# Optimization experiments

Hardware: AMD Instinct MI355X
Metric: run time of the kernel (lower is better)

The kernel has to match this reference:

```python
import jax, jax.numpy as jnp
import numpy as np

D_MODEL = 1024
N_HEADS = 16
D_KEYS = 64
GROUP_POSITIONS = [list(range(g * 32, (g + 1) * 32)) for g in range(4)]


def _make_tables(group_positions, dim):
    # InGroup table: pe[j,i] = (j/Lg) * L0 / 10000^(2*(i//2)/dim)
    L0 = len(group_positions[0])
    rows = []
    for grp in group_positions:
        Lg = len(grp)
        for j in range(Lg):
            rows.append([j / Lg * L0 / np.power(10000.0, 2 * (i // 2) / dim) for i in range(dim)])
    pe = np.array(rows)
    ingroup = np.concatenate([np.sin(pe[:, 0::2]), np.cos(pe[:, 1::2])], axis=1).astype(np.float32)
    # Sequence (group) table: pe[j,i] = grp[0] / 10000^(j/Lg), constant over i
    rows = []
    for grp in group_positions:
        Lg = len(grp)
        for j in range(Lg):
            rows.append([grp[0] / np.power(10000.0, j / Lg) for _ in range(dim)])
    pe = np.array(rows)
    seq = np.concatenate([np.sin(pe[:, 0::2]), np.cos(pe[:, 1::2])], axis=1).astype(np.float32)
    return jnp.asarray(ingroup), jnp.asarray(seq)


def setup_inputs() -> dict:
    key = jax.random.key(0)
    ks = jax.random.split(key, 12)
    B, L, S = 64, 128, 128
    dqk = D_KEYS * N_HEADS
    sc_in = 1.0 / np.sqrt(D_MODEL)
    sc_out = 1.0 / np.sqrt(dqk)
    inp = {
        "queries": jax.random.normal(ks[0], (B, L, D_MODEL), jnp.float32),
        "keys": jax.random.normal(ks[1], (B, S, D_MODEL), jnp.float32),
        "values": jax.random.normal(ks[2], (B, S, D_MODEL), jnp.float32),
        "attn_mask": jnp.zeros((B, 1, L, S), dtype=bool),
        "Wq": jax.random.normal(ks[3], (D_MODEL, dqk), jnp.float32) * sc_in,
        "bq": jnp.zeros((dqk,), jnp.float32),
        "Wk": jax.random.normal(ks[4], (D_MODEL, dqk), jnp.float32) * sc_in,
        "bk": jnp.zeros((dqk,), jnp.float32),
        "Wv": jax.random.normal(ks[5], (D_MODEL, dqk), jnp.float32) * sc_in,
        "bv": jnp.zeros((dqk,), jnp.float32),
        "Wo": jax.random.normal(ks[6], (dqk, D_MODEL), jnp.float32) * sc_out,
        "bo": jnp.zeros((D_MODEL,), jnp.float32),
    }
    pos_ingroup, pos_seq = _make_tables(GROUP_POSITIONS, D_KEYS)
    inp["pos_ingroup"] = pos_ingroup  # [n_pos, d_keys]
    inp["pos_seq"] = pos_seq          # [n_pos, d_keys]
    return inp


def _rope(x, pos):
    # x: [B, H, L, D]; pos: [L, D]
    sin, cos = jnp.split(pos, 2, axis=-1)
    sin_pos = jnp.stack([sin, sin], axis=-1).reshape(pos.shape)
    cos_pos = jnp.stack([cos, cos], axis=-1).reshape(pos.shape)
    rot = jnp.stack([-x[..., 1::2], x[..., ::2]], axis=-1).reshape(x.shape)
    return x * cos_pos + rot * sin_pos


def reference(queries, keys, values, attn_mask, Wq, bq, Wk, bk, Wv, bv, Wo, bo, pos_ingroup, pos_seq):
    B, L, _ = queries.shape
    S = keys.shape[1]
    H, E = N_HEADS, D_KEYS
    q = (queries @ Wq + bq).reshape(B, L, H, E).transpose(0, 2, 1, 3)  # [B,H,L,E]
    k = (keys @ Wk + bk).reshape(B, S, H, E).transpose(0, 2, 1, 3)
    v = (values @ Wv + bv).reshape(B, S, H, E).transpose(0, 2, 1, 3)
    # group-sequence in-group RoPE, then group RoPE (tables gathered at arange positions)
    q = _rope(_rope(q, pos_ingroup[:L]), pos_seq[:L])
    k = _rope(_rope(k, pos_ingroup[:S]), pos_seq[:S])
    # inner full attention on [B,L,H,E] layout
    scale = 1.0 / jnp.sqrt(jnp.asarray(E, q.dtype))
    scores = jnp.einsum("bhle,bhse->bhls", q, k) * scale
    scores = jnp.where(attn_mask, jnp.asarray(-jnp.inf, scores.dtype), scores)
    attn = jax.nn.softmax(scores, axis=-1)  # [B,H,L,S]
    out = jnp.einsum("bhls,bhsd->blhd", attn, v).reshape(B, L, H * E)
    return out @ Wo + bo, attn
```

## Files before the change

### kernel.cpp

```cpp
#include <hip/hip_runtime.h>
#include <cstdint>

typedef float f32x4 __attribute__((ext_vector_type(4)));
typedef __bf16 bf16x8 __attribute__((ext_vector_type(8)));

typedef __attribute__((address_space(3))) uint32_t lds_u32;
typedef __attribute__((address_space(1))) const uint32_t glb_u32;

#define GLOAD_LDS16(gp, lp) \
  __builtin_amdgcn_global_load_lds((glb_u32*)(uintptr_t)(gp), (lds_u32*)(uintptr_t)(lp), 16, 0, 0)

__device__ inline unsigned short f2bf(float f) {
  union { float f; uint32_t u; } v; v.f = f;
  uint32_t u = v.u;
  return (unsigned short)((u + 0x7fffu + ((u >> 16) & 1u)) >> 16);
}

__global__ void prep_w(const float* __restrict__ wq, const float* __restrict__ wk,
                       const float* __restrict__ wv, const float* __restrict__ wo,
                       unsigned short* __restrict__ wt)
{
  __shared__ float t[64][65];
  const int z = blockIdx.z;
  const float* W = (z == 0) ? wq : (z == 1) ? wk : (z == 2) ? wv : wo;
  unsigned short* Wt = wt + (size_t)z * 1048576;
  const int n0 = blockIdx.x * 64, k0 = blockIdx.y * 64;
  const int tx = threadIdx.x & 63, ty = threadIdx.x >> 6;
#pragma unroll
  for (int i = 0; i < 16; i++) {
    int row = i * 4 + ty;
    t[row][tx] = W[(size_t)(k0 + row) * 1024 + n0 + tx];
  }
  __syncthreads();
#pragma unroll
  for (int i = 0; i < 16; i++) {
    int row = i * 4 + ty;
    Wt[(size_t)(n0 + row) * 1024 + k0 + tx] = f2bf(t[tx][row]);
  }
}

__global__ void comb_kernel(const float* __restrict__ ing, const float* __restrict__ seq,
                            float* __restrict__ cosc, float* __restrict__ sinc)
{
  int idx = blockIdx.x * 256 + threadIdx.x;
  int j = idx >> 5, i = idx & 31;
  float s1 = ing[j * 64 + i], c1 = ing[j * 64 + 32 + i];
  float s2 = seq[j * 64 + i], c2 = seq[j * 64 + 32 + i];
  cosc[idx] = c1 * c2 - s1 * s2;
  sinc[idx] = s1 * c2 + c1 * s2;
}

__global__ void cvt_kernel(const float* __restrict__ q, const float* __restrict__ k,
                           const float* __restrict__ v, unsigned short* __restrict__ dst)
{
  const int z = blockIdx.z;
  const float* src = (z == 0) ? q : (z == 1) ? k : v;
  unsigned short* d = dst + (size_t)z * 8388608;
  size_t i = ((size_t)blockIdx.x * 256 + threadIdx.x) * 4;
  float4 f = *(const float4*)&src[i];
  ushort4 o;
  o.x = f2bf(f.x); o.y = f2bf(f.y); o.z = f2bf(f.z); o.w = f2bf(f.w);
  *(ushort4*)&d[i] = o;
}

__global__ __launch_bounds__(256, 2)
void gemm_bt(const unsigned short* __restrict__ Abase,
             const unsigned short* __restrict__ Bbase,
             const float* __restrict__ b0, const float* __restrict__ b1,
             const float* __restrict__ b2,
             unsigned short* __restrict__ qb, unsigned short* __restrict__ kb,
             unsigned short* __restrict__ vtb,
             float* __restrict__ outf,
             const float* __restrict__ cosc, const float* __restrict__ sinc,
             int final_mode)
{
  __shared__ __attribute__((aligned(16))) unsigned short As[128 * 64];
  __shared__ __attribute__((aligned(16))) unsigned short Bs[128 * 64];

  const int tid = threadIdx.x;
  const int lane = tid & 63;
  const int wave = tid >> 6;
  const int quad = lane >> 4;
  const int l15 = lane & 15;

  const int z = blockIdx.z;
  const int tileM = blockIdx.x * 128;
  const int tileN = blockIdx.y * 128;
  const int K = 1024;

  const unsigned short* A = Abase + (size_t)z * (8192u * 1024u);
  const unsigned short* B = Bbase + (size_t)z * (1024u * 1024u);

  const int wm = (wave >> 1) * 64;
  const int wn = (wave & 1) * 64;

  f32x4 acc[4][4];
#pragma unroll
  for (int a = 0; a < 4; a++)
#pragma unroll
    for (int n = 0; n < 4; n++)
      acc[a][n] = (f32x4){0.f, 0.f, 0.f, 0.f};

  for (int k0 = 0; k0 < K; k0 += 64) {
#pragma unroll
    for (int cc = 0; cc < 4; cc++) {
      int c = wave * 4 + cc;
      int s = c * 64 + lane;
      int row = s >> 3;
      int gc = (s & 7) ^ (row & 7);
      const unsigned short* ga = A + (size_t)(tileM + row) * K + k0 + gc * 8;
      const unsigned short* gb = B + (size_t)(tileN + row) * K + k0 + gc * 8;
      GLOAD_LDS16(ga, &As[c * 512]);
      GLOAD_LDS16(gb, &Bs[c * 512]);
    }
    __syncthreads();

#pragma unroll
    for (int ks = 0; ks < 2; ks++) {
      bf16x8 af[4], bfr[4];
#pragma unroll
      for (int a = 0; a < 4; a++) {
        int r = wm + a * 16 + l15;
        int cp = (ks * 4 + quad) ^ (r & 7);
        af[a] = *(const bf16x8*)&As[(r * 8 + cp) * 8];
      }
#pragma unroll
      for (int n = 0; n < 4; n++) {
        int r = wn + n * 16 + l15;
        int cp = (ks * 4 + quad) ^ (r & 7);
        bfr[n] = *(const bf16x8*)&Bs[(r * 8 + cp) * 8];
      }
#pragma unroll
      for (int a = 0; a < 4; a++)
#pragma unroll
        for (int n = 0; n < 4; n++)
          acc[a][n] = __builtin_amdgcn_mfma_f32_16x16x32_bf16(af[a], bfr[n], acc[a][n], 0, 0, 0);
    }
    __syncthreads();
  }

  if (final_mode) {
#pragma unroll
    for (int n = 0; n < 4; n++) {
      int cg = tileN + wn + n * 16 + l15;
      float bias = b0[cg];
#pragma unroll
      for (int a = 0; a < 4; a++)
#pragma unroll
        for (int reg = 0; reg < 4; reg++) {
          int r = tileM + wm + a * 16 + quad * 4 + reg;
          outf[(size_t)r * 1024 + cg] = acc[a][n][reg] + bias;
        }
    }
  } else {
    const float* bias = (z == 0) ? b0 : (z == 1) ? b1 : b2;
    unsigned short* outq = (z == 0) ? qb : kb;
#pragma unroll
    for (int n = 0; n < 4; n++) {
      int cg = tileN + wn + n * 16 + l15;
      float bv_ = bias[cg];
      int h = cg >> 6, e = cg & 63;
#pragma unroll
      for (int a = 0; a < 4; a++)
#pragma unroll
        for (int reg = 0; reg < 4; reg++) {
          int r = tileM + wm + a * 16 + quad * 4 + reg;
          int bb = r >> 7, l = r & 127;
          float v = acc[a][n][reg] + bv_;
          if (z == 2) {
            vtb[(((size_t)bb * 16 + h) * 64 + e) * 128 + l] = f2bf(v);
          } else {
            float other = __shfl_xor(v, 1);
            float cs = cosc[l * 32 + (e >> 1)];
            float sn = sinc[l * 32 + (e >> 1)];
            float res = v * cs + ((e & 1) ? other : -other) * sn;
            outq[(((size_t)bb * 16 + h) * 128 + l) * 64 + e] = f2bf(res);
          }
        }
    }
  }
}

__global__ __launch_bounds__(256, 2)
void attn_kernel(const unsigned short* __restrict__ qb,
                 const unsigned short* __restrict__ kb,
                 const unsigned short* __restrict__ vtb,
                 const unsigned char* __restrict__ mask,
                 float* __restrict__ attn_out,
                 unsigned short* __restrict__ ob)
{
  __shared__ __attribute__((aligned(16))) unsigned short Pb[128 * 136];
  const int tid = threadIdx.x;
  const int lane = tid & 63;
  const int wave = tid >> 6;
  const int quad = lane >> 4;
  const int l15 = lane & 15;
  const int bh = blockIdx.x;
  const int b = bh >> 4;
  const int h = bh & 15;

  const unsigned short* q = qb + (size_t)bh * 128 * 64;
  const unsigned short* k = kb + (size_t)bh * 128 * 64;
  const unsigned short* vt = vtb + (size_t)bh * 64 * 128;

  f32x4 sacc[2][8];
#pragma unroll
  for (int mt = 0; mt < 2; mt++)
#pragma unroll
    for (int nt = 0; nt < 8; nt++)
      sacc[mt][nt] = (f32x4){0.f, 0.f, 0.f, 0.f};

#pragma unroll
  for (int ks = 0; ks < 2; ks++) {
    bf16x8 aq[2], bk[8];
#pragma unroll
    for (int mt = 0; mt < 2; mt++)
      aq[mt] = *(const bf16x8*)&q[(size_t)(wave * 32 + mt * 16 + l15) * 64 + ks * 32 + quad * 8];
#pragma unroll
    for (int nt = 0; nt < 8; nt++)
      bk[nt] = *(const bf16x8*)&k[(size_t)(nt * 16 + l15) * 64 + ks * 32 + quad * 8];
#pragma unroll
    for (int mt = 0; mt < 2; mt++)
#pragma unroll
      for (int nt = 0; nt < 8; nt++)
        sacc[mt][nt] = __builtin_amdgcn_mfma_f32_16x16x32_bf16(aq[mt], bk[nt], sacc[mt][nt], 0, 0, 0);
  }

  const float scale = 0.125f;
#pragma unroll
  for (int mt = 0; mt < 2; mt++) {
#pragma unroll
    for (int reg = 0; reg < 4; reg++) {
      int r = wave * 32 + mt * 16 + quad * 4 + reg;
      const unsigned char* mrow = mask + ((size_t)b * 128 + r) * 128;
      float sv[8];
#pragma unroll
      for (int nt = 0; nt < 8; nt++) {
        float x = sacc[mt][nt][reg] * scale;
        if (mrow[nt * 16 + l15]) x = -__builtin_inff();
        sv[nt] = x;
      }
      float m = sv[0];
#pragma unroll
      for (int nt = 1; nt < 8; nt++) m = fmaxf(m, sv[nt]);
#pragma unroll
      for (int off = 1; off < 16; off <<= 1) m = fmaxf(m, __shfl_xor(m, off));
      float s = 0.f;
#pragma unroll
      for (int nt = 0; nt < 8; nt++) { sv[nt] = __expf(sv[nt] - m); s += sv[nt]; }
#pragma unroll
      for (int off = 1; off < 16; off <<= 1) s += __shfl_xor(s, off);
      float inv = 1.0f / s;
      float* arow = attn_out + ((size_t)bh * 128 + r) * 128;
#pragma unroll
      for (int nt = 0; nt < 8; nt++) {
        float p = sv[nt] * inv;
        arow[nt * 16 + l15] = p;
        Pb[r * 136 + nt * 16 + l15] = f2bf(p);
      }
    }
  }
  __syncthreads();

  f32x4 oacc[2][4];
#pragma unroll
  for (int mt = 0; mt < 2; mt++)
#pragma unroll
    for (int nt = 0; nt < 4; nt++)
      oacc[mt][nt] = (f32x4){0.f, 0.f, 0.f, 0.f};

#pragma unroll
  for (int ks = 0; ks < 4; ks++) {
    bf16x8 bv[4], ap[2];
#pragma unroll
    for (int nt = 0; nt < 4; nt++)
      bv[nt] = *(const bf16x8*)&vt[(size_t)(nt * 16 + l15) * 128 + ks * 32 + quad * 8];
#pragma unroll
    for (int mt = 0; mt < 2; mt++)
      ap[mt] = *(const bf16x8*)&Pb[(size_t)(wave * 32 + mt * 16 + l15) * 136 + ks * 32 + quad * 8];
#pragma unroll
    for (int mt = 0; mt < 2; mt++)
#pragma unroll
      for (int nt = 0; nt < 4; nt++)
        oacc[mt][nt] = __builtin_amdgcn_mfma_f32_16x16x32_bf16(ap[mt], bv[nt], oacc[mt][nt], 0, 0, 0);
  }

#pragma unroll
  for (int mt = 0; mt < 2; mt++)
#pragma unroll
    for (int nt = 0; nt < 4; nt++)
#pragma unroll
      for (int reg = 0; reg < 4; reg++) {
        int r = wave * 32 + mt * 16 + quad * 4 + reg;
        int e = nt * 16 + l15;
        ob[((size_t)b * 128 + r) * 1024 + h * 64 + e] = f2bf(oacc[mt][nt][reg]);
      }
}

extern "C" void kernel_launch(void* const* d_in, const int* in_sizes, int n_in,
                              void* d_out, int out_size, void* d_ws, size_t ws_size,
                              hipStream_t stream)
{
  const float* queries = (const float*)d_in[0];
  const float* keys    = (const float*)d_in[1];
  const float* values  = (const float*)d_in[2];
  const unsigned char* mask = (const unsigned char*)d_in[3];
  const float* Wq = (const float*)d_in[4];
  const float* bq = (const float*)d_in[5];
  const float* Wk = (const float*)d_in[6];
  const float* bk = (const float*)d_in[7];
  const float* Wv = (const float*)d_in[8];
  const float* bv = (const float*)d_in[9];
  const float* Wo = (const float*)d_in[10];
  const float* bo = (const float*)d_in[11];
  const float* ping = (const float*)d_in[12];
  const float* pseq = (const float*)d_in[13];

  float* out  = (float*)d_out;
  float* attn = out + 8388608;
  unsigned short* Xbf = (unsigned short*)attn;

  char* ws = (char*)d_ws;
  unsigned short* Wt  = (unsigned short*)(ws);
  float* cosc = (float*)(ws + 8388608);
  float* sinc = (float*)(ws + 8388608 + 16384);
  unsigned short* qbuf = (unsigned short*)(ws + 8421376);
  unsigned short* kbuf = (unsigned short*)(ws + 8421376 + 16777216);
  unsigned short* vtbuf= (unsigned short*)(ws + 8421376 + 2*16777216);
  unsigned short* obuf = (unsigned short*)(ws + 8421376 + 3*16777216);

  prep_w<<<dim3(16, 16, 4), 256, 0, stream>>>(Wq, Wk, Wv, Wo, Wt);
  comb_kernel<<<16, 256, 0, stream>>>(ping, pseq, cosc, sinc);
  cvt_kernel<<<dim3(8192, 1, 3), 256, 0, stream>>>(queries, keys, values, Xbf);
  gemm_bt<<<dim3(64, 8, 3), 256, 0, stream>>>(Xbf, Wt, bq, bk, bv,
                                              qbuf, kbuf, vtbuf, nullptr,
                                              cosc, sinc, 0);
  attn_kernel<<<dim3(1024), 256, 0, stream>>>(qbuf, kbuf, vtbuf, mask, attn, obuf);
  gemm_bt<<<dim3(64, 8, 1), 256, 0, stream>>>(obuf, Wt + 3 * 1048576, bo, bo, bo,
                                              qbuf, kbuf, vtbuf, out,
                                              cosc, sinc, 1);
}
```

Before: 351.7 us.

## Fuse fp32-to-bf16 input conversion into QKV GEMM and split attention rows per block

Removes the separate conversion kernel: the QKV GEMM now loads fp32 activations directly through registers with a one-tile-ahead prefetch, packs them to bf16 with a cheap truncation-style rounding, and writes them into swizzled LDS. This drops a full fp32 read plus bf16 write and re-read of the three input tensors. The attention kernel is split so each block handles half the query rows, doubling the grid and halving LDS. The attention-probability and final-output stores become nontemporal. The register prefetch raises register pressure in the GEMM, and the packing rounds half-up instead of to nearest-even, a slight numeric change.

Measured after the change: 363.6 us. +3.4%, slower.

```diff
diff --git a/kernel.cpp b/kernel.cpp
--- a/kernel.cpp
+++ b/kernel.cpp
@@ -14,6 +14,11 @@
   union { float f; uint32_t u; } v; v.f = f;
   uint32_t u = v.u;
   return (unsigned short)((u + 0x7fffu + ((u >> 16) & 1u)) >> 16);
+}
+
+__device__ inline uint32_t pkbf(float a, float b) {
+  union { float f; uint32_t u; } x, y; x.f = a; y.f = b;
+  return __builtin_amdgcn_perm(y.u + 0x8000u, x.u + 0x8000u, 0x07060302u);
 }
 
 __global__ void prep_w(const float* __restrict__ wq, const float* __restrict__ wk,
@@ -50,29 +55,15 @@
   sinc[idx] = s1 * c2 + c1 * s2;
 }
 
-__global__ void cvt_kernel(const float* __restrict__ q, const float* __restrict__ k,
-                           const float* __restrict__ v, unsigned short* __restrict__ dst)
-{
-  const int z = blockIdx.z;
-  const float* src = (z == 0) ? q : (z == 1) ? k : v;
-  unsigned short* d = dst + (size_t)z * 8388608;
-  size_t i = ((size_t)blockIdx.x * 256 + threadIdx.x) * 4;
-  float4 f = *(const float4*)&src[i];
-  ushort4 o;
-  o.x = f2bf(f.x); o.y = f2bf(f.y); o.z = f2bf(f.z); o.w = f2bf(f.w);
-  *(ushort4*)&d[i] = o;
-}
-
 __global__ __launch_bounds__(256, 2)
-void gemm_bt(const unsigned short* __restrict__ Abase,
-             const unsigned short* __restrict__ Bbase,
-             const float* __restrict__ b0, const float* __restrict__ b1,
-             const float* __restrict__ b2,
-             unsigned short* __restrict__ qb, unsigned short* __restrict__ kb,
-             unsigned short* __restrict__ vtb,
-             float* __restrict__ outf,
-             const float* __restrict__ cosc, const float* __restrict__ sinc,
-             int final_mode)
+void gemm_qkv(const float* __restrict__ qf, const float* __restrict__ kf,
+              const float* __restrict__ vf,
+              const unsigned short* __restrict__ Bbase,
+              const float* __restrict__ b0, const float* __restrict__ b1,
+              const float* __restrict__ b2,
+              unsigned short* __restrict__ qb, unsigned short* __restrict__ kb,
+              unsigned short* __restrict__ vtb,
+              const float* __restrict__ cosc, const float* __restrict__ sinc)
 {
   __shared__ __attribute__((aligned(16))) unsigned short As[128 * 64];
   __shared__ __attribute__((aligned(16))) unsigned short Bs[128 * 64];
@@ -86,13 +77,14 @@
   const int z = blockIdx.z;
   const int tileM = blockIdx.x * 128;
   const int tileN = blockIdx.y * 128;
-  const int K = 1024;
-
-  const unsigned short* A = Abase + (size_t)z * (8192u * 1024u);
+
+  const float* A = (z == 0) ? qf : (z == 1) ? kf : vf;
   const unsigned short* B = Bbase + (size_t)z * (1024u * 1024u);
 
   const int wm = (wave >> 1) * 64;
   const int wn = (wave & 1) * 64;
+  const int arow = lane >> 3;
+  const int ag = lane & 7;
 
   f32x4 acc[4][4];
 #pragma unroll
@@ -101,19 +93,47 @@
     for (int n = 0; n < 4; n++)
       acc[a][n] = (f32x4){0.f, 0.f, 0.f, 0.f};
 
-  for (int k0 = 0; k0 < K; k0 += 64) {
+  float4 pre[4][2];
+  {
+    const float* Ab = A + (size_t)(tileM + arow) * 1024 + ag * 8;
+#pragma unroll
+    for (int cc = 0; cc < 4; cc++) {
+      const float* ga = Ab + (size_t)((wave * 4 + cc) * 8) * 1024;
+      pre[cc][0] = *(const float4*)ga;
+      pre[cc][1] = *(const float4*)(ga + 4);
+    }
+  }
+
+  for (int k0 = 0; k0 < 1024; k0 += 64) {
 #pragma unroll
     for (int cc = 0; cc < 4; cc++) {
       int c = wave * 4 + cc;
       int s = c * 64 + lane;
       int row = s >> 3;
       int gc = (s & 7) ^ (row & 7);
-      const unsigned short* ga = A + (size_t)(tileM + row) * K + k0 + gc * 8;
-      const unsigned short* gb = B + (size_t)(tileN + row) * K + k0 + gc * 8;
-      GLOAD_LDS16(ga, &As[c * 512]);
-      GLOAD_LDS16(gb, &Bs[c * 512]);
+      GLOAD_LDS16(B + (size_t)(tileN + row) * 1024 + k0 + gc * 8, &Bs[c * 512]);
+    }
+#pragma unroll
+    for (int cc = 0; cc < 4; cc++) {
+      int row = (wave * 4 + cc) * 8 + arow;
+      uint32_t w0 = pkbf(pre[cc][0].x, pre[cc][0].y);
+      uint32_t w1 = pkbf(pre[cc][0].z, pre[cc][0].w);
+      uint32_t w2 = pkbf(pre[cc][1].x, pre[cc][1].y);
+      uint32_t w3 = pkbf(pre[cc][1].z, pre[cc][1].w);
+      uint4 wv = make_uint4(w0, w1, w2, w3);
+      *(uint4*)&As[(row * 8 + (ag ^ (row & 7))) * 8] = wv;
     }
     __syncthreads();
+
+    if (k0 + 64 < 1024) {
+      const float* Ab = A + (size_t)(tileM + arow) * 1024 + (k0 + 64) + ag * 8;
+#pragma unroll
+      for (int cc = 0; cc < 4; cc++) {
+        const float* ga = Ab + (size_t)((wave * 4 + cc) * 8) * 1024;
+        pre[cc][0] = *(const float4*)ga;
+        pre[cc][1] = *(const float4*)(ga + 4);
+      }
+    }
 
 #pragma unroll
     for (int ks = 0; ks < 2; ks++) {
@@ -139,45 +159,107 @@
     __syncthreads();
   }
 
-  if (final_mode) {
-#pragma unroll
-    for (int n = 0; n < 4; n++) {
-      int cg = tileN + wn + n * 16 + l15;
-      float bias = b0[cg];
+  const float* bias = (z == 0) ? b0 : (z == 1) ? b1 : b2;
+  unsigned short* outq = (z == 0) ? qb : kb;
+#pragma unroll
+  for (int n = 0; n < 4; n++) {
+    int cg = tileN + wn + n * 16 + l15;
+    float bv_ = bias[cg];
+    int h = cg >> 6, e = cg & 63;
+#pragma unroll
+    for (int a = 0; a < 4; a++)
+#pragma unroll
+      for (int reg = 0; reg < 4; reg++) {
+        int r = tileM + wm + a * 16 + quad * 4 + reg;
+        int bb = r >> 7, l = r & 127;
+        float v = acc[a][n][reg] + bv_;
+        if (z == 2) {
+          vtb[(((size_t)bb * 16 + h) * 64 + e) * 128 + l] = f2bf(v);
+        } else {
+          float other = __shfl_xor(v, 1);
+          float cs = cosc[l * 32 + (e >> 1)];
+          float sn = sinc[l * 32 + (e >> 1)];
+          float res = v * cs + ((e & 1) ? other : -other) * sn;
+          outq[(((size_t)bb * 16 + h) * 128 + l) * 64 + e] = f2bf(res);
+        }
+      }
+  }
+}
+
+__global__ __launch_bounds__(256, 2)
+void gemm_out(const unsigned short* __restrict__ A,
+              const unsigned short* __restrict__ B,
+              const float* __restrict__ bo,
+              float* __restrict__ outf)
+{
+  __shared__ __attribute__((aligned(16))) unsigned short As[128 * 64];
+  __shared__ __attribute__((aligned(16))) unsigned short Bs[128 * 64];
+
+  const int tid = threadIdx.x;
+  const int lane = tid & 63;
+  const int wave = tid >> 6;
+  const int quad = lane >> 4;
+  const int l15 = lane & 15;
+
+  const int tileM = blockIdx.x * 128;
+  const int tileN = blockIdx.y * 128;
+
+  const int wm = (wave >> 1) * 64;
+  const int wn = (wave & 1) * 64;
+
+  f32x4 acc[4][4];
+#pragma unroll
+  for (int a = 0; a < 4; a++)
+#pragma unroll
+    for (int n = 0; n < 4; n++)
+      acc[a][n] = (f32x4){0.f, 0.f, 0.f, 0.f};
+
+  for (int k0 = 0; k0 < 1024; k0 += 64) {
+#pragma unroll
+    for (int cc = 0; cc < 4; cc++) {
+      int c = wave * 4 + cc;
+      int s = c * 64 + lane;
+      int row = s >> 3;
+      int gc = (s & 7) ^ (row & 7);
+      GLOAD_LDS16(A + (size_t)(tileM + row) * 1024 + k0 + gc * 8, &As[c * 512]);
+      GLOAD_LDS16(B + (size_t)(tileN + row) * 1024 + k0 + gc * 8, &Bs[c * 512]);
+    }
+    __syncthreads();
+#pragma unroll
+    for (int ks = 0; ks < 2; ks++) {
+      bf16x8 af[4], bfr[4];
+#pragma unroll
+      for (int a = 0; a < 4; a++) {
+        int r = wm + a * 16 + l15;
+        int cp = (ks * 4 + quad) ^ (r & 7);
+        af[a] = *(const bf16x8*)&As[(r * 8 + cp) * 8];
+      }
+#pragma unroll
+      for (int n = 0; n < 4; n++) {
+        int r = wn + n * 16 + l15;
+        int cp = (ks * 4 + quad) ^ (r & 7);
+        bfr[n] = *(const bf16x8*)&Bs[(r * 8 + cp) * 8];
+      }
 #pragma unroll
       for (int a = 0; a < 4; a++)
 #pragma unroll
-        for (int reg = 0; reg < 4; reg++) {
-          int r = tileM + wm + a * 16 + quad * 4 + reg;
-          outf[(size_t)r * 1024 + cg] = acc[a][n][reg] + bias;
-        }
-    }
-  } else {
-    const float* bias = (z == 0) ? b0 : (z == 1) ? b1 : b2;
-    unsigned short* outq = (z == 0) ? qb : kb;
-#pragma unroll
-    for (int n = 0; n < 4; n++) {
-      int cg = tileN + wn + n * 16 + l15;
-      float bv_ = bias[cg];
-      int h = cg >> 6, e = cg & 63;
-#pragma unroll
-      for (int a = 0; a < 4; a++)
-#pragma unroll
-        for (int reg = 0; reg < 4; reg++) {
-          int r = tileM + wm + a * 16 + quad * 4 + reg;
-          int bb = r >> 7, l = r & 127;
-          float v = acc[a][n][reg] + bv_;
-          if (z == 2) {
-            vtb[(((size_t)bb * 16 + h) * 64 + e) * 128 + l] = f2bf(v);
-          } else {
-            float other = __shfl_xor(v, 1);
-            float cs = cosc[l * 32 + (e >> 1)];
-            float sn = sinc[l * 32 + (e >> 1)];
-            float res = v * cs + ((e & 1) ? other : -other) * sn;
-            outq[(((size_t)bb * 16 + h) * 128 + l) * 64 + e] = f2bf(res);
-          }
-        }
-    }
+        for (int n = 0; n < 4; n++)
+          acc[a][n] = __builtin_amdgcn_mfma_f32_16x16x32_bf16(af[a], bfr[n], acc[a][n], 0, 0, 0);
+    }
+    __syncthreads();
+  }
+
+#pragma unroll
+  for (int n = 0; n < 4; n++) {
+    int cg = tileN + wn + n * 16 + l15;
+    float bias = bo[cg];
+#pragma unroll
+    for (int a = 0; a < 4; a++)
+#pragma unroll
+      for (int reg = 0; reg < 4; reg++) {
+        int r = tileM + wm + a * 16 + quad * 4 + reg;
+        __builtin_nontemporal_store(acc[a][n][reg] + bias, &outf[(size_t)r * 1024 + cg]);
+      }
   }
 }
 
@@ -189,112 +271,99 @@
                  float* __restrict__ attn_out,
                  unsigned short* __restrict__ ob)
 {
-  __shared__ __attribute__((aligned(16))) unsigned short Pb[128 * 136];
+  __shared__ __attribute__((aligned(16))) unsigned short Pb[64 * 136];
   const int tid = threadIdx.x;
   const int lane = tid & 63;
   const int wave = tid >> 6;
   const int quad = lane >> 4;
   const int l15 = lane & 15;
-  const int bh = blockIdx.x;
+  const int blk = blockIdx.x;
+  const int bh = blk >> 1;
+  const int half = blk & 1;
   const int b = bh >> 4;
   const int h = bh & 15;
+  const int r0 = half * 64;
 
   const unsigned short* q = qb + (size_t)bh * 128 * 64;
   const unsigned short* k = kb + (size_t)bh * 128 * 64;
   const unsigned short* vt = vtb + (size_t)bh * 64 * 128;
 
-  f32x4 sacc[2][8];
-#pragma unroll
-  for (int mt = 0; mt < 2; mt++)
-#pragma unroll
-    for (int nt = 0; nt < 8; nt++)
-      sacc[mt][nt] = (f32x4){0.f, 0.f, 0.f, 0.f};
+  f32x4 sacc[8];
+#pragma unroll
+  for (int nt = 0; nt < 8; nt++)
+    sacc[nt] = (f32x4){0.f, 0.f, 0.f, 0.f};
 
 #pragma unroll
   for (int ks = 0; ks < 2; ks++) {
-    bf16x8 aq[2], bk[8];
-#pragma unroll
-    for (int mt = 0; mt < 2; mt++)
-      aq[mt] = *(const bf16x8*)&q[(size_t)(wave * 32 + mt * 16 + l15) * 64 + ks * 32 + quad * 8];
+    bf16x8 aq = *(const bf16x8*)&q[(size_t)(r0 + wave * 16 + l15) * 64 + ks * 32 + quad * 8];
+    bf16x8 bk[8];
 #pragma unroll
     for (int nt = 0; nt < 8; nt++)
       bk[nt] = *(const bf16x8*)&k[(size_t)(nt * 16 + l15) * 64 + ks * 32 + quad * 8];
 #pragma unroll
-    for (int mt = 0; mt < 2; mt++)
-#pragma unroll
-      for (int nt = 0; nt < 8; nt++)
-        sacc[mt][nt] = __builtin_amdgcn_mfma_f32_16x16x32_bf16(aq[mt], bk[nt], sacc[mt][nt], 0, 0, 0);
+    for (int nt = 0; nt < 8; nt++)
+      sacc[nt] = __builtin_amdgcn_mfma_f32_16x16x32_bf16(aq, bk[nt], sacc[nt], 0, 0, 0);
   }
 
   const float scale = 0.125f;
 #pragma unroll
-  for (int mt = 0; mt < 2; mt++) {
-#pragma unroll
-    for (int reg = 0; reg < 4; reg++) {
-      int r = wave * 32 + mt * 16 + quad * 4 + reg;
-      const unsigned char* mrow = mask + ((size_t)b * 128 + r) * 128;
-      float sv[8];
-#pragma unroll
-      for (int nt = 0; nt < 8; nt++) {
-        float x = sacc[mt][nt][reg] * scale;
-        if (mrow[nt * 16 + l15]) x = -__builtin_inff();
-        sv[nt] = x;
-      }
-      float m = sv[0];
-#pragma unroll
-      for (int nt = 1; nt < 8; nt++) m = fmaxf(m, sv[nt]);
-#pragma unroll
-      for (int off = 1; off < 16; off <<= 1) m = fmaxf(m, __shfl_xor(m, off));
-      float s = 0.f;
-#pragma unroll
-      for (int nt = 0; nt < 8; nt++) { sv[nt] = __expf(sv[nt] - m); s += sv[nt]; }
-#pragma unroll
-      for (int off = 1; off < 16; off <<= 1) s += __shfl_xor(s, off);
-      float inv = 1.0f / s;
-      float* arow = attn_out + ((size_t)bh * 128 + r) * 128;
-#pragma unroll
-      for (int nt = 0; nt < 8; nt++) {
-        float p = sv[nt] * inv;
-        arow[nt * 16 + l15] = p;
-        Pb[r * 136 + nt * 16 + l15] = f2bf(p);
-      }
+  for (int reg = 0; reg < 4; reg++) {
+    int rl = wave * 16 + quad * 4 + reg;
+    int gr = r0 + rl;
+    const unsigned char* mrow = mask + ((size_t)b * 128 + gr) * 128;
+    float sv[8];
+#pragma unroll
+    for (int nt = 0; nt < 8; nt++) {
+      float x = sacc[nt][reg] * scale;
+      if (mrow[nt * 16 + l15]) x = -__builtin_inff();
+      sv[nt] = x;
+    }
+    float m = sv[0];
+#pragma unroll
+    for (int nt = 1; nt < 8; nt++) m = fmaxf(m, sv[nt]);
+#pragma unroll
+    for (int off = 1; off < 16; off <<= 1) m = fmaxf(m, __shfl_xor(m, off));
+    float s = 0.f;
+#pragma unroll
+    for (int nt = 0; nt < 8; nt++) { sv[nt] = __expf(sv[nt] - m); s += sv[nt]; }
+#pragma unroll
+    for (int off = 1; off < 16; off <<= 1) s += __shfl_xor(s, off);
+    float inv = 1.0f / s;
+    float* arow = attn_out + ((size_t)bh * 128 + gr) * 128;
+#pragma unroll
+    for (int nt = 0; nt < 8; nt++) {
+      float p = sv[nt] * inv;
+      __builtin_nontemporal_store(p, &arow[nt * 16 + l15]);
+      Pb[rl * 136 + nt * 16 + l15] = f2bf(p);
     }
   }
   __syncthreads();
 
-  f32x4 oacc[2][4];
-#pragma unroll
-  for (int mt = 0; mt < 2; mt++)
-#pragma unroll
-    for (int nt = 0; nt < 4; nt++)
-      oacc[mt][nt] = (f32x4){0.f, 0.f, 0.f, 0.f};
+  f32x4 oacc[4];
+#pragma unroll
+  for (int nt = 0; nt < 4; nt++)
+    oacc[nt] = (f32x4){0.f, 0.f, 0.f, 0.f};
 
 #pragma unroll
   for (int ks = 0; ks < 4; ks++) {
-    bf16x8 bv[4], ap[2];
+    bf16x8 ap = *(const bf16x8*)&Pb[(size_t)(wave * 16 + l15) * 136 + ks * 32 + quad * 8];
+    bf16x8 bv[4];
 #pragma unroll
     for (int nt = 0; nt < 4; nt++)
       bv[nt] = *(const bf16x8*)&vt[(size_t)(nt * 16 + l15) * 128 + ks * 32 + quad * 8];
 #pragma unroll
-    for (int mt = 0; mt < 2; mt++)
-      ap[mt] = *(const bf16x8*)&Pb[(size_t)(wave * 32 + mt * 16 + l15) * 136 + ks * 32 + quad * 8];
-#pragma unroll
-    for (int mt = 0; mt < 2; mt++)
-#pragma unroll
-      for (int nt = 0; nt < 4; nt++)
-        oacc[mt][nt] = __builtin_amdgcn_mfma_f32_16x16x32_bf16(ap[mt], bv[nt], oacc[mt][nt], 0, 0, 0);
-  }
-
-#pragma unroll
-  for (int mt = 0; mt < 2; mt++)
-#pragma unroll
     for (int nt = 0; nt < 4; nt++)
-#pragma unroll
-      for (int reg = 0; reg < 4; reg++) {
-        int r = wave * 32 + mt * 16 + quad * 4 + reg;
-        int e = nt * 16 + l15;
-        ob[((size_t)b * 128 + r) * 1024 + h * 64 + e] = f2bf(oacc[mt][nt][reg]);
-      }
+      oacc[nt] = __builtin_amdgcn_mfma_f32_16x16x32_bf16(ap, bv[nt], oacc[nt], 0, 0, 0);
+  }
+
+#pragma unroll
+  for (int nt = 0; nt < 4; nt++)
+#pragma unroll
+    for (int reg = 0; reg < 4; reg++) {
+      int gr = r0 + wave * 16 + quad * 4 + reg;
+      int e = nt * 16 + l15;
+      ob[((size_t)b * 128 + gr) * 1024 + h * 64 + e] = f2bf(oacc[nt][reg]);
+    }
 }
 
 extern "C" void kernel_launch(void* const* d_in, const int* in_sizes, int n_in,
@@ -318,7 +387,6 @@
 
   float* out  = (float*)d_out;
   float* attn = out + 8388608;
-  unsigned short* Xbf = (unsigned short*)attn;
 
   char* ws = (char*)d_ws;
   unsigned short* Wt  = (unsigned short*)(ws);
@@ -331,12 +399,9 @@
 
   prep_w<<<dim3(16, 16, 4), 256, 0, stream>>>(Wq, Wk, Wv, Wo, Wt);
   comb_kernel<<<16, 256, 0, stream>>>(ping, pseq, cosc, sinc);
-  cvt_kernel<<<dim3(8192, 1, 3), 256, 0, stream>>>(queries, keys, values, Xbf);
-  gemm_bt<<<dim3(64, 8, 3), 256, 0, stream>>>(Xbf, Wt, bq, bk, bv,
-                                              qbuf, kbuf, vtbuf, nullptr,
-                                              cosc, sinc, 0);
-  attn_kernel<<<dim3(1024), 256, 0, stream>>>(qbuf, kbuf, vtbuf, mask, attn, obuf);
-  gemm_bt<<<dim3(64, 8, 1), 256, 0, stream>>>(obuf, Wt + 3 * 1048576, bo, bo, bo,
-                                              qbuf, kbuf, vtbuf, out,
-                                              cosc, sinc, 1);
-}
+  gemm_qkv<<<dim3(64, 8, 3), 256, 0, stream>>>(queries, keys, values, Wt,
+                                               bq, bk, bv,
+                                               qbuf, kbuf, vtbuf, cosc, sinc);
+  attn_kernel<<<dim3(2048), 256, 0, stream>>>(qbuf, kbuf, vtbuf, mask, attn, obuf);
+  gemm_out<<<dim3(64, 8), 256, 0, stream>>>(obuf, Wt + 3 * 1048576, bo, out);
+}
```
